# Optimization experiments

Measured on AMD Instinct MI355X. Metric: run time of the kernel, lower is better.

## Reference

```python
import jax, jax.numpy as jnp
import numpy as np

NE = 64        # num experts
H = 1024       # hidden_size
F = 2048       # ffn_hidden_size per expert
T = 16384      # total tokens


def setup_inputs() -> dict:
    key = jax.random.key(0)
    k1, k2, k3 = jax.random.split(key, 3)
    x = jax.random.normal(k1, (T, H), jnp.float32)
    w1 = jax.random.normal(k2, (NE, F, H), jnp.float32) * 0.02
    w2 = jax.random.normal(k3, (NE, F, H), jnp.float32) * 0.02
    # ragged token counts per expert, summing exactly to T
    rng = np.random.default_rng(0)
    sizes = rng.multinomial(T, np.ones(NE) / NE)
    tokens_per_expert = jnp.asarray(sizes, jnp.int32)
    return {"x": x, "w1": w1, "w2": w2, "tokens_per_expert": tokens_per_expert}


def _grouped_gmm(x, w, sizes, trans_b=False):
    # grouped GEMM: per-expert segment of x multiplied by that expert's weight.
    # sizes are concrete host ints (group boundaries are static), so we emit
    # one GEMM per expert with static slices, matching gg.ops.gmm semantics.
    offs = np.concatenate([[0], np.cumsum(sizes)]).astype(np.int64)
    outs = []
    for e in range(len(sizes)):
        xe = x[int(offs[e]):int(offs[e + 1])]          # [n_e, k]
        we = w[e].T if trans_b else w[e]               # [k, n]
        outs.append(xe @ we)
    return jnp.concatenate(outs, axis=0)


def reference(x, w1, w2, tokens_per_expert):
    sizes = np.asarray(tokens_per_expert)
    h = _grouped_gmm(x, w1, sizes, trans_b=True)       # [T, F]
    h = jax.nn.gelu(h, approximate=False)              # torch F.gelu (exact erf)
    return _grouped_gmm(h, w2, sizes, trans_b=False)   # [T, H]
```

## Files before the change

### kernel.cpp

```cpp
#include <hip/hip_runtime.h>
#include <hip/hip_bf16.h>

#define NE 64
#define HDIM 1024
#define FDIM 2048
#define TDIM 16384

typedef __attribute__((ext_vector_type(8))) short short8;
typedef __attribute__((ext_vector_type(4))) float f32x4;
typedef unsigned short u16;
typedef unsigned int u32;

struct IC0 { static constexpr int v = 0; };
struct IC1 { static constexpr int v = 1; };

__device__ __forceinline__ u16 f2bf(float f) {
  return __bfloat16_as_ushort(__float2bfloat16(f));
}
__device__ __forceinline__ u32 pk2(float a, float b) {
  return (u32)f2bf(a) | ((u32)f2bf(b) << 16);
}
template<int N> __device__ __forceinline__ void waitv() {
  if constexpr (N == 4)       asm volatile("s_waitcnt vmcnt(4)" ::: "memory");
  else if constexpr (N == 6)  asm volatile("s_waitcnt vmcnt(6)" ::: "memory");
  else if constexpr (N == 8)  asm volatile("s_waitcnt vmcnt(8)" ::: "memory");
  else if constexpr (N == 10) asm volatile("s_waitcnt vmcnt(10)" ::: "memory");
}
__device__ __forceinline__ void waitl() {
  asm volatile("s_waitcnt lgkmcnt(0)" ::: "memory");
}

__global__ void k_prep(const int* __restrict__ tpe, int4* __restrict__ map,
                       int* __restrict__ nblocks) {
  if (threadIdx.x != 0 || blockIdx.x != 0) return;
  int off = 0, nb = 0;
  for (int e = 0; e < NE; ++e) {
    int n = tpe[e];
    for (int r = 0; r < n; r += 128) {
      int re = (r + 128 < n) ? (r + 128) : n;
      map[nb++] = make_int4(e, off + r, off + re, 0);
    }
    off += n;
  }
  *nblocks = nb;
}

__global__ void k_conv(const float4* __restrict__ in, uint2* __restrict__ out, int n4) {
  int stride = gridDim.x * blockDim.x;
  for (int i = blockIdx.x * blockDim.x + threadIdx.x; i < n4; i += stride) {
    float4 v = in[i];
    uint2 o;
    o.x = pk2(v.x, v.y);
    o.y = pk2(v.z, v.w);
    out[i] = o;
  }
}

template<int K, int N, bool GELU, int BMODE>
__global__ __launch_bounds__(256) void k_gemm(
    const u16* __restrict__ A, const float* __restrict__ Bf, void* __restrict__ C,
    const int4* __restrict__ map, const int* __restrict__ nblocks)
{
  if ((int)blockIdx.x >= *nblocks) return;
  const int4 mi = map[blockIdx.x];
  const int e = mi.x, row0 = mi.y, rowend = mi.z;
  const int n0 = blockIdx.y << 7;
  const int NT = K / 32;
  constexpr int LB = (BMODE == 1) ? 4 : 8;

  __shared__ u16 sa[2][4096];
  __shared__ u16 sb[128 * 40];

  const int tid = threadIdx.x;
  const int wid = tid >> 6, lane = tid & 63;
  const int wr = wid >> 1, wc = wid & 1;
  const int fr = lane & 15, fq = lane >> 4;

  f32x4 acc[4][4];
#pragma unroll
  for (int m = 0; m < 4; ++m)
#pragma unroll
    for (int n = 0; n < 4; ++n) acc[m][n] = (f32x4)0.f;

  const float* B = Bf + (size_t)e * ((size_t)N * K);

  float4 rb1[2][4];
  float2 rb2[2][8];
  const int np2 = (tid & 63) << 1;
  const int oct = tid >> 6;

  auto issueA = [&](int t) {
    const int buf = t & 1;
#pragma unroll
    for (int i = 0; i < 2; ++i) {
      int slot = i * 256 + tid;
      int row = row0 + (slot >> 2);
      row = row < TDIM ? row : TDIM - 1;
      const u16* g = A + (size_t)row * K + t * 32 + (slot & 3) * 8;
      __builtin_amdgcn_global_load_lds(
          (const __attribute__((address_space(1))) u32*)g,
          (__attribute__((address_space(3))) u32*)(&sa[buf][i * 2048 + wid * 512]),
          16, 0, 0);
    }
  };
  auto loadB = [&](int t, auto ic) {
    constexpr int S = decltype(ic)::v;
    if constexpr (BMODE == 1) {
#pragma unroll
      for (int i = 0; i < 4; ++i) {
        int slot = i * 256 + tid;
        rb1[S][i] = *(const float4*)(B + (size_t)(n0 + (slot >> 3)) * K + t * 32 + (slot & 7) * 4);
      }
    } else {
      const float* src = B + (size_t)(t * 32 + oct * 8) * N + n0 + np2;
#pragma unroll
      for (int i = 0; i < 8; ++i) rb2[S][i] = *(const float2*)(src + (size_t)i * N);
    }
  };
  auto writeB = [&](auto ic) {
    constexpr int S = decltype(ic)::v;
    if constexpr (BMODE == 1) {
#pragma unroll
      for (int i = 0; i < 4; ++i) {
        int slot = i * 256 + tid;
        uint2 o;
        o.x = pk2(rb1[S][i].x, rb1[S][i].y);
        o.y = pk2(rb1[S][i].z, rb1[S][i].w);
        *(uint2*)(&sb[(slot >> 3) * 40 + (slot & 7) * 4]) = o;
      }
    } else {
      uint4 c0, c1;
      c0.x = pk2(rb2[S][0].x, rb2[S][1].x); c0.y = pk2(rb2[S][2].x, rb2[S][3].x);
      c0.z = pk2(rb2[S][4].x, rb2[S][5].x); c0.w = pk2(rb2[S][6].x, rb2[S][7].x);
      c1.x = pk2(rb2[S][0].y, rb2[S][1].y); c1.y = pk2(rb2[S][2].y, rb2[S][3].y);
      c1.z = pk2(rb2[S][4].y, rb2[S][5].y); c1.w = pk2(rb2[S][6].y, rb2[S][7].y);
      *(uint4*)(&sb[np2 * 40 + oct * 8]) = c0;
      *(uint4*)(&sb[(np2 + 1) * 40 + oct * 8]) = c1;
    }
  };

  auto body = [&](int t, auto icCur) {
    waitv<2 + LB>();
    waitl();
    __builtin_amdgcn_s_barrier();
    const int cur = t & 1;
    short8 av[4], bv[4];
#pragma unroll
    for (int m = 0; m < 4; ++m)
      av[m] = *(const short8*)(&sa[cur][(wr * 64 + m * 16 + fr) * 32 + fq * 8]);
#pragma unroll
    for (int n = 0; n < 4; ++n)
      bv[n] = *(const short8*)(&sb[(wc * 64 + n * 16 + fr) * 40 + fq * 8]);
    waitl();
    __builtin_amdgcn_sched_barrier(0);
    __builtin_amdgcn_s_barrier();
    if (t + 2 < NT) issueA(t + 2);
    if (t + 1 < NT) writeB(icCur);
    if (t + 3 < NT) loadB(t + 3, icCur);
    __builtin_amdgcn_sched_barrier(0);
#pragma unroll
    for (int m = 0; m < 4; ++m)
#pragma unroll
      for (int n = 0; n < 4; ++n)
        acc[m][n] = __builtin_amdgcn_mfma_f32_16x16x32_bf16(av[m], bv[n], acc[m][n], 0, 0, 0);
  };

  issueA(0);
  loadB(0, IC0{});
  loadB(1, IC1{});
  waitv<LB>();
  writeB(IC0{});
  issueA(1);
  loadB(2, IC0{});
  for (int t = 0; t < NT; t += 2) {
    body(t, IC1{});
    body(t + 1, IC0{});
  }

#pragma unroll
  for (int m = 0; m < 4; ++m) {
    const int rb = row0 + wr * 64 + m * 16 + fq * 4;
#pragma unroll
    for (int n = 0; n < 4; ++n) {
      const int col = n0 + wc * 64 + n * 16 + fr;
#pragma unroll
      for (int j = 0; j < 4; ++j) {
        int r = rb + j;
        if (r < rowend) {
          float vv = acc[m][n][j];
          if constexpr (GELU) {
            vv = 0.5f * vv * (1.f + erff(vv * 0.70710678118654752f));
            ((u16*)C)[(size_t)r * N + col] = f2bf(vv);
          } else {
            ((float*)C)[(size_t)r * N + col] = vv;
          }
        }
      }
    }
  }
}

extern "C" void kernel_launch(void* const* d_in, const int* in_sizes, int n_in,
                              void* d_out, int out_size, void* d_ws, size_t ws_size,
                              hipStream_t stream) {
  const float* x  = (const float*)d_in[0];
  const float* w1 = (const float*)d_in[1];
  const float* w2 = (const float*)d_in[2];
  const int*  tpe = (const int*)d_in[3];

  char* ws = (char*)d_ws;
  int4* map     = (int4*)ws;
  int*  nblocks = (int*)(ws + 4096);
  u16*  xb      = (u16*)(ws + 8192);
  u16*  hb      = xb + (size_t)TDIM * HDIM;

  k_prep<<<1, 64, 0, stream>>>(tpe, map, nblocks);
  k_conv<<<2048, 256, 0, stream>>>((const float4*)x, (uint2*)xb, (TDIM * HDIM) / 4);
  k_gemm<HDIM, FDIM, true,  1><<<dim3(192, FDIM / 128), 256, 0, stream>>>(
      xb, w1, (void*)hb, map, nblocks);
  k_gemm<FDIM, HDIM, false, 2><<<dim3(192, HDIM / 128), 256, 0, stream>>>(
      hb, w2, d_out, map, nblocks);
}
```

Before: 555.0 us.

## Double the grouped-GEMM M tile to 256 rows with 512-thread blocks

Doubles the M tile from 128 to 256 rows per block: 8 waves over 512 threads, twice the shared A buffer, and B loads redistributed across the extra threads. Each expert's fp32 weight tile is then re-read and converted to bf16 fewer times, which should cut the dominant weight traffic. The 2D grid becomes a 1D grid in which consecutive blocks share the same row block and differ only in N tile. The cost is more padded compute when an expert's last row block is only partly filled, and fewer, larger blocks in flight.

```diff
diff --git a/kernel.cpp b/kernel.cpp
--- a/kernel.cpp
+++ b/kernel.cpp
@@ -21,8 +21,8 @@
   return (u32)f2bf(a) | ((u32)f2bf(b) << 16);
 }
 template<int N> __device__ __forceinline__ void waitv() {
-  if constexpr (N == 4)       asm volatile("s_waitcnt vmcnt(4)" ::: "memory");
-  else if constexpr (N == 6)  asm volatile("s_waitcnt vmcnt(6)" ::: "memory");
+  if constexpr (N == 2)       asm volatile("s_waitcnt vmcnt(2)" ::: "memory");
+  else if constexpr (N == 4)  asm volatile("s_waitcnt vmcnt(4)" ::: "memory");
   else if constexpr (N == 8)  asm volatile("s_waitcnt vmcnt(8)" ::: "memory");
   else if constexpr (N == 10) asm volatile("s_waitcnt vmcnt(10)" ::: "memory");
 }
@@ -36,8 +36,8 @@
   int off = 0, nb = 0;
   for (int e = 0; e < NE; ++e) {
     int n = tpe[e];
-    for (int r = 0; r < n; r += 128) {
-      int re = (r + 128 < n) ? (r + 128) : n;
+    for (int r = 0; r < n; r += 256) {
+      int re = (r + 256 < n) ? (r + 256) : n;
       map[nb++] = make_int4(e, off + r, off + re, 0);
     }
     off += n;
@@ -56,20 +56,22 @@
   }
 }
 
-template<int K, int N, bool GELU, int BMODE>
-__global__ __launch_bounds__(256) void k_gemm(
+template<int K, int N, bool GELU, int BMODE, int NY>
+__global__ __launch_bounds__(512) void k_gemm(
     const u16* __restrict__ A, const float* __restrict__ Bf, void* __restrict__ C,
     const int4* __restrict__ map, const int* __restrict__ nblocks)
 {
-  if ((int)blockIdx.x >= *nblocks) return;
-  const int4 mi = map[blockIdx.x];
+  const int mblk = (int)blockIdx.x / NY;
+  const int nblk = (int)blockIdx.x % NY;
+  if (mblk >= *nblocks) return;
+  const int4 mi = map[mblk];
   const int e = mi.x, row0 = mi.y, rowend = mi.z;
-  const int n0 = blockIdx.y << 7;
+  const int n0 = nblk << 7;
   const int NT = K / 32;
-  constexpr int LB = (BMODE == 1) ? 4 : 8;
-
-  __shared__ u16 sa[2][4096];
-  __shared__ u16 sb[128 * 40];
+  constexpr int LB = (BMODE == 1) ? 2 : 8;
+
+  __shared__ __align__(16) u16 sa[2][8192];
+  __shared__ __align__(16) u16 sb[128 * 40];
 
   const int tid = threadIdx.x;
   const int wid = tid >> 6, lane = tid & 63;
@@ -84,22 +86,22 @@
 
   const float* B = Bf + (size_t)e * ((size_t)N * K);
 
-  float4 rb1[2][4];
-  float2 rb2[2][8];
-  const int np2 = (tid & 63) << 1;
-  const int oct = tid >> 6;
+  float4 rb1[2][2];
+  float  rb2[2][8];
+  const int bn  = tid & 127;
+  const int oct = tid >> 7;
 
   auto issueA = [&](int t) {
     const int buf = t & 1;
 #pragma unroll
     for (int i = 0; i < 2; ++i) {
-      int slot = i * 256 + tid;
+      int slot = i * 512 + tid;
       int row = row0 + (slot >> 2);
       row = row < TDIM ? row : TDIM - 1;
       const u16* g = A + (size_t)row * K + t * 32 + (slot & 3) * 8;
       __builtin_amdgcn_global_load_lds(
           (const __attribute__((address_space(1))) u32*)g,
-          (__attribute__((address_space(3))) u32*)(&sa[buf][i * 2048 + wid * 512]),
+          (__attribute__((address_space(3))) u32*)(&sa[buf][i * 4096 + wid * 512]),
           16, 0, 0);
     }
   };
@@ -107,35 +109,32 @@
     constexpr int S = decltype(ic)::v;
     if constexpr (BMODE == 1) {
 #pragma unroll
-      for (int i = 0; i < 4; ++i) {
-        int slot = i * 256 + tid;
+      for (int i = 0; i < 2; ++i) {
+        int slot = i * 512 + tid;
         rb1[S][i] = *(const float4*)(B + (size_t)(n0 + (slot >> 3)) * K + t * 32 + (slot & 7) * 4);
       }
     } else {
-      const float* src = B + (size_t)(t * 32 + oct * 8) * N + n0 + np2;
-#pragma unroll
-      for (int i = 0; i < 8; ++i) rb2[S][i] = *(const float2*)(src + (size_t)i * N);
+      const float* src = B + (size_t)(t * 32 + oct * 8) * N + n0 + bn;
+#pragma unroll
+      for (int i = 0; i < 8; ++i) rb2[S][i] = src[(size_t)i * N];
     }
   };
   auto writeB = [&](auto ic) {
     constexpr int S = decltype(ic)::v;
     if constexpr (BMODE == 1) {
 #pragma unroll
-      for (int i = 0; i < 4; ++i) {
-        int slot = i * 256 + tid;
+      for (int i = 0; i < 2; ++i) {
+        int slot = i * 512 + tid;
         uint2 o;
         o.x = pk2(rb1[S][i].x, rb1[S][i].y);
         o.y = pk2(rb1[S][i].z, rb1[S][i].w);
         *(uint2*)(&sb[(slot >> 3) * 40 + (slot & 7) * 4]) = o;
       }
     } else {
-      uint4 c0, c1;
-      c0.x = pk2(rb2[S][0].x, rb2[S][1].x); c0.y = pk2(rb2[S][2].x, rb2[S][3].x);
-      c0.z = pk2(rb2[S][4].x, rb2[S][5].x); c0.w = pk2(rb2[S][6].x, rb2[S][7].x);
-      c1.x = pk2(rb2[S][0].y, rb2[S][1].y); c1.y = pk2(rb2[S][2].y, rb2[S][3].y);
-      c1.z = pk2(rb2[S][4].y, rb2[S][5].y); c1.w = pk2(rb2[S][6].y, rb2[S][7].y);
-      *(uint4*)(&sb[np2 * 40 + oct * 8]) = c0;
-      *(uint4*)(&sb[(np2 + 1) * 40 + oct * 8]) = c1;
+      uint4 c;
+      c.x = pk2(rb2[S][0], rb2[S][1]); c.y = pk2(rb2[S][2], rb2[S][3]);
+      c.z = pk2(rb2[S][4], rb2[S][5]); c.w = pk2(rb2[S][6], rb2[S][7]);
+      *(uint4*)(&sb[bn * 40 + oct * 8]) = c;
     }
   };
 
@@ -216,8 +215,8 @@
 
   k_prep<<<1, 64, 0, stream>>>(tpe, map, nblocks);
   k_conv<<<2048, 256, 0, stream>>>((const float4*)x, (uint2*)xb, (TDIM * HDIM) / 4);
-  k_gemm<HDIM, FDIM, true,  1><<<dim3(192, FDIM / 128), 256, 0, stream>>>(
+  k_gemm<HDIM, FDIM, true,  1, 16><<<128 * 16, 512, 0, stream>>>(
       xb, w1, (void*)hb, map, nblocks);
-  k_gemm<FDIM, HDIM, false, 2><<<dim3(192, HDIM / 128), 256, 0, stream>>>(
+  k_gemm<FDIM, HDIM, false, 2, 8><<<128 * 8, 512, 0, stream>>>(
       hb, w2, d_out, map, nblocks);
 }
```

Result: faster. 540.5 us (-2.6%).
